# Kernel optimization log

Hardware: AMD Instinct MI355X
Metric: run time of the kernel (lower is better)

Reference implementation:

```python
import jax, jax.numpy as jnp
import numpy as np


def _feature_map(x):
    # elu(x) + 1, the canonical positive feature map for linear attention
    return jax.nn.elu(x) + 1.0


def setup_inputs() -> dict:
    key = jax.random.key(0)
    kq, kk, kv = jax.random.split(key, 3)
    B, T, H, D, M = 2, 2048, 8, 64, 64
    q = jax.random.normal(kq, (B, T, H, D), dtype=jnp.float32)
    k = jax.random.normal(kk, (B, T, H, D), dtype=jnp.float32)
    v = jax.random.normal(kv, (B, T, H, M), dtype=jnp.float32)
    return {"q": q, "k": k, "v": v}


def reference(q, k, v):
    # q,k: [B,T,H,D]; v: [B,T,H,M]
    qf = _feature_map(q)
    kf = _feature_map(k)
    # running sum of keys over time (causal)
    k_sum = jnp.cumsum(kf, axis=1)                      # [B,T,H,D]
    z = 1.0 / jnp.einsum('bthd,bthd->bth', qf, k_sum)   # [B,T,H]
    # outer products k_i v_i^T; NOTE: original torch code cumsums over dim=-2
    # (the D axis of the [B,T,H,D,M] tensor), reproduced faithfully here.
    kv = jnp.einsum('bthd,bthm->bthdm', kf, v)           # [B,T,H,D,M]
    kv_sum = jnp.cumsum(kv, axis=-2)                     # cumsum over D, per source
    out = jnp.einsum('bthd,bthdm,bth->bthm', qf, kv_sum, z)
    return out
```

## Files before the change

### kernel.cpp

```cpp
#include <hip/hip_runtime.h>

#define BB 2
#define TT 2048
#define HH 8
#define DD 64
#define CC 128
#define TC (TT / CC)
#define NI 4
#define STRIDE (HH * DD)
#define NBH (BB * HH)

__device__ __forceinline__ float feat(float x) {
    return x > 0.f ? x + 1.f : __expf(x);
}

__device__ __forceinline__ void feat4(float4& a) {
    a.x = feat(a.x); a.y = feat(a.y); a.z = feat(a.z); a.w = feat(a.w);
}

__device__ __forceinline__ void segscan(float4& a, int seg) {
    float u;
    u = __shfl_up(a.x, 16, 64); if (seg >= 1) a.x += u;
    u = __shfl_up(a.y, 16, 64); if (seg >= 1) a.y += u;
    u = __shfl_up(a.z, 16, 64); if (seg >= 1) a.z += u;
    u = __shfl_up(a.w, 16, 64); if (seg >= 1) a.w += u;
    u = __shfl_up(a.x, 32, 64); if (seg >= 2) a.x += u;
    u = __shfl_up(a.y, 32, 64); if (seg >= 2) a.y += u;
    u = __shfl_up(a.z, 32, 64); if (seg >= 2) a.z += u;
    u = __shfl_up(a.w, 32, 64); if (seg >= 2) a.w += u;
}

__device__ __forceinline__ void xorred4(float4& a) {
    a.x += __shfl_xor(a.x, 16, 64); a.y += __shfl_xor(a.y, 16, 64);
    a.z += __shfl_xor(a.z, 16, 64); a.w += __shfl_xor(a.w, 16, 64);
    a.x += __shfl_xor(a.x, 32, 64); a.y += __shfl_xor(a.y, 32, 64);
    a.z += __shfl_xor(a.z, 32, 64); a.w += __shfl_xor(a.w, 32, 64);
}


__global__ void __launch_bounds__(64)
chunk_sums_kernel(const float* __restrict__ k, float* __restrict__ ws) {
    const int idx  = blockIdx.x;
    const int c    = idx & (CC - 1);
    const int h    = (idx >> 7) & (HH - 1);
    const int b    = idx >> 10;
    const int lane = threadIdx.x;
    const int g    = lane & 15;
    const int seg  = lane >> 4;

    const size_t off0 = (((size_t)b * TT + c * TC + seg) * HH + h) * DD + g * 4;
    float4 s = make_float4(0.f, 0.f, 0.f, 0.f);
    #pragma unroll
    for (int i = 0; i < NI; ++i) {
        const float4 kv = *(const float4*)(k + off0 + (size_t)(4 * i) * STRIDE);
        s.x += feat(kv.x); s.y += feat(kv.y); s.z += feat(kv.z); s.w += feat(kv.w);
    }
    xorred4(s);
    if (seg == 0)
        *(float4*)(ws + (size_t)idx * DD + g * 4) = s;
}

__global__ void __launch_bounds__(64)
linattn_kernel(const float* __restrict__ q, const float* __restrict__ k,
               const float* __restrict__ v, const float* __restrict__ ws,
               float* __restrict__ out) {
    const int idx  = blockIdx.x;
    const int c    = idx & (CC - 1);
    const int h    = (idx >> 7) & (HH - 1);
    const int b    = idx >> 10;
    const int lane = threadIdx.x;
    const int g    = lane & 15;
    const int seg  = lane >> 4;

    const size_t off0 = (((size_t)b * TT + c * TC + seg) * HH + h) * DD + g * 4;

    float4 kf[NI], qf[NI], vv[NI];
    #pragma unroll
    for (int i = 0; i < NI; ++i) {
        const size_t o = off0 + (size_t)(4 * i) * STRIDE;
        kf[i] = *(const float4*)(k + o);
        qf[i] = *(const float4*)(q + o);
        vv[i] = *(const float4*)(v + o);
    }

    const float* wsg = ws + (size_t)(idx - c) * DD + g * 4;
    float4 carry = make_float4(0.f, 0.f, 0.f, 0.f);
    for (int cp = seg; cp < c; cp += 4) {
        const float4 t = *(const float4*)(wsg + (size_t)cp * DD);
        carry.x += t.x; carry.y += t.y; carry.z += t.z; carry.w += t.w;
    }
    xorred4(carry);

    #pragma unroll
    for (int i = 0; i < NI; ++i) { feat4(kf[i]); feat4(qf[i]); }

    float4 base = carry;
    #pragma unroll
    for (int i = 0; i < NI; ++i) {
        float4 inc = kf[i];
        segscan(inc, seg);
        float4 run;
        run.x = base.x + inc.x; run.y = base.y + inc.y;
        run.z = base.z + inc.z; run.w = base.w + inc.w;
        if (i < NI - 1) {
            base.x += __shfl(inc.x, 48 + g, 64);
            base.y += __shfl(inc.y, 48 + g, 64);
            base.z += __shfl(inc.z, 48 + g, 64);
            base.w += __shfl(inc.w, 48 + g, 64);
        }

        float4 p;
        p.x = kf[i].x; p.y = p.x + kf[i].y; p.z = p.y + kf[i].z; p.w = p.z + kf[i].w;
        float cg = p.w;
        #pragma unroll
        for (int o = 1; o <= 8; o <<= 1) {
            const float u = __shfl_up(cg, o, 16);
            if (g >= o) cg += u;
        }
        const float e  = cg - p.w;
        const float sq = qf[i].x + qf[i].y + qf[i].z + qf[i].w;
        float s1 = qf[i].x * p.x + qf[i].y * p.y + qf[i].z * p.z + qf[i].w * p.w
                 + e * sq;
        float s2 = qf[i].x * run.x + qf[i].y * run.y + qf[i].z * run.z
                 + qf[i].w * run.w;
        #pragma unroll
        for (int o = 1; o <= 8; o <<= 1) {
            s1 += __shfl_xor(s1, o, 64);
            s2 += __shfl_xor(s2, o, 64);
        }

        const float r = s1 * __builtin_amdgcn_rcpf(s2);
        float4 ov;
        ov.x = vv[i].x * r; ov.y = vv[i].y * r;
        ov.z = vv[i].z * r; ov.w = vv[i].w * r;
        *(float4*)(out + off0 + (size_t)(4 * i) * STRIDE) = ov;
    }
}

extern "C" void kernel_launch(void* const* d_in, const int* in_sizes, int n_in,
                              void* d_out, int out_size, void* d_ws, size_t ws_size,
                              hipStream_t stream) {
    const float* q = (const float*)d_in[0];
    const float* k = (const float*)d_in[1];
    const float* v = (const float*)d_in[2];
    float* out = (float*)d_out;
    float* ws  = (float*)d_ws;

    const int nblk = BB * HH * CC;
    chunk_sums_kernel<<<nblk, 64, 0, stream>>>(k, ws);
    linattn_kernel<<<nblk, 64, 0, stream>>>(q, k, v, ws, out);
}
```

Measured before the change: 86.55 us.

## Add dedicated chunk-prefix scan kernel and shrink chunks to four timesteps

Replaces the per-block serial carry accumulation (each block summing up to 127 prior chunk sums) with a separate prefix kernel that computes exclusive prefix sums of chunk totals once per batch-head. Chunk size drops from 16 to 4 timesteps, so the main kernel processes one float4 per lane with no inner loop, and grid sizes grow accordingly. This removes redundant quadratic carry reads but adds a third launch and a serialized 16-block prefix kernel with low parallelism.

Result: faster. 78.86 us (-8.9%).

```diff
diff --git a/kernel.cpp b/kernel.cpp
--- a/kernel.cpp
+++ b/kernel.cpp
@@ -4,11 +4,11 @@
 #define TT 2048
 #define HH 8
 #define DD 64
-#define CC 128
+#define CC 512
 #define TC (TT / CC)
-#define NI 4
 #define STRIDE (HH * DD)
 #define NBH (BB * HH)
+#define PW (CC / 16)
 
 __device__ __forceinline__ float feat(float x) {
     return x > 0.f ? x + 1.f : __expf(x);
@@ -16,18 +16,6 @@
 
 __device__ __forceinline__ void feat4(float4& a) {
     a.x = feat(a.x); a.y = feat(a.y); a.z = feat(a.z); a.w = feat(a.w);
-}
-
-__device__ __forceinline__ void segscan(float4& a, int seg) {
-    float u;
-    u = __shfl_up(a.x, 16, 64); if (seg >= 1) a.x += u;
-    u = __shfl_up(a.y, 16, 64); if (seg >= 1) a.y += u;
-    u = __shfl_up(a.z, 16, 64); if (seg >= 1) a.z += u;
-    u = __shfl_up(a.w, 16, 64); if (seg >= 1) a.w += u;
-    u = __shfl_up(a.x, 32, 64); if (seg >= 2) a.x += u;
-    u = __shfl_up(a.y, 32, 64); if (seg >= 2) a.y += u;
-    u = __shfl_up(a.z, 32, 64); if (seg >= 2) a.z += u;
-    u = __shfl_up(a.w, 32, 64); if (seg >= 2) a.w += u;
 }
 
 __device__ __forceinline__ void xorred4(float4& a) {
@@ -41,23 +29,53 @@
 __global__ void __launch_bounds__(64)
 chunk_sums_kernel(const float* __restrict__ k, float* __restrict__ ws) {
     const int idx  = blockIdx.x;
-    const int c    = idx & (CC - 1);
-    const int h    = (idx >> 7) & (HH - 1);
-    const int b    = idx >> 10;
+    const int p    = idx & 255;
+    const int h    = (idx >> 8) & (HH - 1);
+    const int b    = idx >> 11;
+    const int bh   = idx >> 8;
     const int lane = threadIdx.x;
     const int g    = lane & 15;
     const int seg  = lane >> 4;
 
-    const size_t off0 = (((size_t)b * TT + c * TC + seg) * HH + h) * DD + g * 4;
-    float4 s = make_float4(0.f, 0.f, 0.f, 0.f);
+    const size_t off0 = (((size_t)b * TT + p * 8 + seg) * HH + h) * DD + g * 4;
+    float4 k0 = *(const float4*)(k + off0);
+    float4 k1 = *(const float4*)(k + off0 + (size_t)4 * STRIDE);
+
+    feat4(k0); feat4(k1);
+    xorred4(k0);
+    xorred4(k1);
+
+    if (seg == 0) {
+        *(float4*)(ws + ((size_t)bh * CC + 2 * p) * DD + g * 4)     = k0;
+        *(float4*)(ws + ((size_t)bh * CC + 2 * p + 1) * DD + g * 4) = k1;
+    }
+}
+
+__global__ void __launch_bounds__(1024)
+prefix_kernel(float* __restrict__ ws) {
+    const int bh   = blockIdx.x;
+    const int lane = threadIdx.x & 63;
+    const int w    = threadIdx.x >> 6;
+
+    size_t base = ((size_t)bh * CC + w * PW) * DD + lane;
+
+    float val[PW];
     #pragma unroll
-    for (int i = 0; i < NI; ++i) {
-        const float4 kv = *(const float4*)(k + off0 + (size_t)(4 * i) * STRIDE);
-        s.x += feat(kv.x); s.y += feat(kv.y); s.z += feat(kv.z); s.w += feat(kv.w);
-    }
-    xorred4(s);
-    if (seg == 0)
-        *(float4*)(ws + (size_t)idx * DD + g * 4) = s;
+    for (int i = 0; i < PW; ++i) val[i] = ws[base + (size_t)i * DD];
+
+    float run = 0.f, excl[PW];
+    #pragma unroll
+    for (int i = 0; i < PW; ++i) { excl[i] = run; run += val[i]; }
+
+    __shared__ float tot[16][DD];
+    tot[w][lane] = run;
+    __syncthreads();
+
+    float carry = 0.f;
+    for (int w2 = 0; w2 < w; ++w2) carry += tot[w2][lane];
+
+    #pragma unroll
+    for (int i = 0; i < PW; ++i) ws[base + (size_t)i * DD] = excl[i] + carry;
 }
 
 __global__ void __launch_bounds__(64)
@@ -66,75 +84,61 @@
                float* __restrict__ out) {
     const int idx  = blockIdx.x;
     const int c    = idx & (CC - 1);
-    const int h    = (idx >> 7) & (HH - 1);
-    const int b    = idx >> 10;
+    const int bh   = idx >> 9;
+    const int h    = bh & (HH - 1);
+    const int b    = bh >> 3;
     const int lane = threadIdx.x;
     const int g    = lane & 15;
     const int seg  = lane >> 4;
 
-    const size_t off0 = (((size_t)b * TT + c * TC + seg) * HH + h) * DD + g * 4;
+    const size_t off = (((size_t)b * TT + c * TC + seg) * HH + h) * DD + g * 4;
 
-    float4 kf[NI], qf[NI], vv[NI];
+    float4 kf = *(const float4*)(k + off);
+    float4 qf = *(const float4*)(q + off);
+    const float4 vv = *(const float4*)(v + off);
+    const float4 carry = *(const float4*)(ws + (size_t)idx * DD + g * 4);
+
+    feat4(kf); feat4(qf);
+
+    float4 i0 = kf;
+    {
+        float u;
+        u = __shfl_up(i0.x, 16, 64); if (seg >= 1) i0.x += u;
+        u = __shfl_up(i0.y, 16, 64); if (seg >= 1) i0.y += u;
+        u = __shfl_up(i0.z, 16, 64); if (seg >= 1) i0.z += u;
+        u = __shfl_up(i0.w, 16, 64); if (seg >= 1) i0.w += u;
+        u = __shfl_up(i0.x, 32, 64); if (seg >= 2) i0.x += u;
+        u = __shfl_up(i0.y, 32, 64); if (seg >= 2) i0.y += u;
+        u = __shfl_up(i0.z, 32, 64); if (seg >= 2) i0.z += u;
+        u = __shfl_up(i0.w, 32, 64); if (seg >= 2) i0.w += u;
+    }
+    float4 run;
+    run.x = carry.x + i0.x; run.y = carry.y + i0.y;
+    run.z = carry.z + i0.z; run.w = carry.w + i0.w;
+
+    float4 p;
+    p.x = kf.x; p.y = p.x + kf.y; p.z = p.y + kf.z; p.w = p.z + kf.w;
+    float cg = p.w;
     #pragma unroll
-    for (int i = 0; i < NI; ++i) {
-        const size_t o = off0 + (size_t)(4 * i) * STRIDE;
-        kf[i] = *(const float4*)(k + o);
-        qf[i] = *(const float4*)(q + o);
-        vv[i] = *(const float4*)(v + o);
+    for (int o = 1; o <= 8; o <<= 1) {
+        const float u = __shfl_up(cg, o, 16);
+        if (g >= o) cg += u;
+    }
+    const float e = cg - p.w;
+
+    const float sq = qf.x + qf.y + qf.z + qf.w;
+    float s1 = qf.x * p.x + qf.y * p.y + qf.z * p.z + qf.w * p.w + e * sq;
+    float s2 = qf.x * run.x + qf.y * run.y + qf.z * run.z + qf.w * run.w;
+    #pragma unroll
+    for (int o = 1; o <= 8; o <<= 1) {
+        s1 += __shfl_xor(s1, o, 64);
+        s2 += __shfl_xor(s2, o, 64);
     }
 
-    const float* wsg = ws + (size_t)(idx - c) * DD + g * 4;
-    float4 carry = make_float4(0.f, 0.f, 0.f, 0.f);
-    for (int cp = seg; cp < c; cp += 4) {
-        const float4 t = *(const float4*)(wsg + (size_t)cp * DD);
-        carry.x += t.x; carry.y += t.y; carry.z += t.z; carry.w += t.w;
-    }
-    xorred4(carry);
-
-    #pragma unroll
-    for (int i = 0; i < NI; ++i) { feat4(kf[i]); feat4(qf[i]); }
-
-    float4 base = carry;
-    #pragma unroll
-    for (int i = 0; i < NI; ++i) {
-        float4 inc = kf[i];
-        segscan(inc, seg);
-        float4 run;
-        run.x = base.x + inc.x; run.y = base.y + inc.y;
-        run.z = base.z + inc.z; run.w = base.w + inc.w;
-        if (i < NI - 1) {
-            base.x += __shfl(inc.x, 48 + g, 64);
-            base.y += __shfl(inc.y, 48 + g, 64);
-            base.z += __shfl(inc.z, 48 + g, 64);
-            base.w += __shfl(inc.w, 48 + g, 64);
-        }
-
-        float4 p;
-        p.x = kf[i].x; p.y = p.x + kf[i].y; p.z = p.y + kf[i].z; p.w = p.z + kf[i].w;
-        float cg = p.w;
-        #pragma unroll
-        for (int o = 1; o <= 8; o <<= 1) {
-            const float u = __shfl_up(cg, o, 16);
-            if (g >= o) cg += u;
-        }
-        const float e  = cg - p.w;
-        const float sq = qf[i].x + qf[i].y + qf[i].z + qf[i].w;
-        float s1 = qf[i].x * p.x + qf[i].y * p.y + qf[i].z * p.z + qf[i].w * p.w
-                 + e * sq;
-        float s2 = qf[i].x * run.x + qf[i].y * run.y + qf[i].z * run.z
-                 + qf[i].w * run.w;
-        #pragma unroll
-        for (int o = 1; o <= 8; o <<= 1) {
-            s1 += __shfl_xor(s1, o, 64);
-            s2 += __shfl_xor(s2, o, 64);
-        }
-
-        const float r = s1 * __builtin_amdgcn_rcpf(s2);
-        float4 ov;
-        ov.x = vv[i].x * r; ov.y = vv[i].y * r;
-        ov.z = vv[i].z * r; ov.w = vv[i].w * r;
-        *(float4*)(out + off0 + (size_t)(4 * i) * STRIDE) = ov;
-    }
+    const float r = s1 * __builtin_amdgcn_rcpf(s2);
+    float4 ov;
+    ov.x = vv.x * r; ov.y = vv.y * r; ov.z = vv.z * r; ov.w = vv.w * r;
+    *(float4*)(out + off) = ov;
 }
 
 extern "C" void kernel_launch(void* const* d_in, const int* in_sizes, int n_in,
@@ -146,7 +150,7 @@
     float* out = (float*)d_out;
     float* ws  = (float*)d_ws;
 
-    const int nblk = BB * HH * CC;
-    chunk_sums_kernel<<<nblk, 64, 0, stream>>>(k, ws);
-    linattn_kernel<<<nblk, 64, 0, stream>>>(q, k, v, ws, out);
+    chunk_sums_kernel<<<NBH * 256, 64, 0, stream>>>(k, ws);
+    prefix_kernel<<<NBH, 1024, 0, stream>>>(ws);
+    linattn_kernel<<<NBH * CC, 64, 0, stream>>>(q, k, v, ws, out);
 }
```
